# Kernel optimization log

Measured on AMD Instinct MI355X. Metric: run time of the kernel, lower is better.

Reference implementation:

```python
import jax, jax.numpy as jnp
import numpy as np

P_SIZE = 5
NUM_HEAD = 8
GN_EPS = 1e-5
LRELU_SLOPE = 0.2


def conv1x1(w, x, b=None):
    # w: [out_c, in_c], x: [n, in_c, h, w]
    y = jnp.einsum('oc,nchw->nohw', w, x)
    if b is not None:
        y = y + b[None, :, None, None]
    return y


def bilinear_sample(feat, sx, sy):
    """grid_sample(mode='bilinear', padding_mode='zeros', align_corners=True).
    With align_corners=True the normalize/denormalize round-trip in
    deformation_grid/grid_sample is the identity, so sx,sy are raw pixel coords.
    feat: [n,c,H,W]; sx,sy: [n,P,H,W] -> out [n,c,P,H,W]."""
    n, c, H, W = feat.shape
    x0 = jnp.floor(sx)
    y0 = jnp.floor(sy)
    x1 = x0 + 1.0
    y1 = y0 + 1.0
    wx1 = sx - x0
    wx0 = 1.0 - wx1
    wy1 = sy - y0
    wy0 = 1.0 - wy1
    feat_flat = feat.reshape(n, c, H * W)

    def corner(xi, yi, wgt):
        valid = (xi >= 0) & (xi <= W - 1) & (yi >= 0) & (yi <= H - 1)
        xc = jnp.clip(xi, 0, W - 1).astype(jnp.int32)
        yc = jnp.clip(yi, 0, H - 1).astype(jnp.int32)
        idx = (yc * W + xc).reshape(n, -1)                      # [n, P*H*W]
        g = jnp.take_along_axis(feat_flat, idx[:, None, :], axis=2)  # [n,c,P*H*W]
        g = g.reshape(n, c, xi.shape[1], H, W)                  # [n,c,P,H,W]
        wm = (wgt * valid.astype(feat.dtype))[:, None]          # [n,1,P,H,W]
        return g * wm

    return (corner(x0, y0, wx0 * wy0) + corner(x1, y0, wx1 * wy0)
            + corner(x0, y1, wx0 * wy1) + corner(x1, y1, wx1 * wy1))


def sample_coords(deform_field, p_size):
    # deform_field: [n,2,h,w] -> absolute pixel coords sx, sy: [n, p^2, h, w]
    n, _, h, w = deform_field.shape
    padding = (p_size - 1) // 2
    shift = jnp.arange(p_size, dtype=deform_field.dtype) - padding
    shift_y, shift_x = jnp.meshgrid(shift, shift, indexing='ij')  # [p,p]
    shift_y = shift_y.reshape(-1, 1, 1)  # [p^2,1,1]
    shift_x = shift_x.reshape(-1, 1, 1)
    gy = jnp.arange(h, dtype=deform_field.dtype)[:, None]  # [h,1]
    gx = jnp.arange(w, dtype=deform_field.dtype)[None, :]  # [1,w]
    sx = gx[None] + shift_x + deform_field[:, None, 0]     # [n,p^2,h,w]
    sy = gy[None] + shift_y + deform_field[:, None, 1]
    return sx, sy


def setup_inputs() -> dict:
    key = jax.random.key(0)
    ks = jax.random.split(key, 12)
    n, c, h, w = 2, 128, 96, 96
    hid = 256
    s = 0.05
    return {
        'query': jax.random.normal(ks[0], (n, c, h, w), jnp.float32),
        'key': jax.random.normal(ks[1], (n, c, h, w), jnp.float32),
        'value': jax.random.normal(ks[2], (n, c, h, w), jnp.float32),
        'deform_field': jax.random.normal(ks[3], (n, 2, h, w), jnp.float32) * 2.0,
        'w_q': jax.random.normal(ks[4], (c, c), jnp.float32) * s,
        'w_k': jax.random.normal(ks[5], (c, c), jnp.float32) * s,
        'w_v': jax.random.normal(ks[6], (c, c), jnp.float32) * s,
        'w_fc': jax.random.normal(ks[7], (c, c), jnp.float32) * s,
        'mlp_w1': jax.random.normal(ks[8], (hid, c), jnp.float32) * s,
        'mlp_b1': jnp.zeros((hid,), jnp.float32),
        'mlp_w2': jax.random.normal(ks[9], (c, hid), jnp.float32) * s,
        'mlp_b2': jnp.zeros((c,), jnp.float32),
        'gn_gamma': jnp.ones((c,), jnp.float32),
        'gn_beta': jnp.zeros((c,), jnp.float32),
    }


def reference(query, key, value, deform_field, w_q, w_k, w_v, w_fc,
              mlp_w1, mlp_b1, mlp_w2, mlp_b2, gn_gamma, gn_beta):
    p2 = P_SIZE * P_SIZE
    n, c, h, w = query.shape
    d_k = c // NUM_HEAD

    q = conv1x1(w_q, query)   # [n,c,h,w]
    k = conv1x1(w_k, key)
    v = conv1x1(w_v, value)

    # deformable window sampling of keys/values
    sx, sy = sample_coords(deform_field, P_SIZE)      # [n,p^2,h,w]
    k_s = bilinear_sample(k, sx, sy)                  # [n,c,p^2,h,w]
    v_s = bilinear_sample(v, sx, sy)

    # split heads
    q = q.reshape(n, NUM_HEAD, d_k, h, w)
    k_s = k_s.reshape(n, NUM_HEAD, d_k, p2, h, w)
    v_s = v_s.reshape(n, NUM_HEAD, d_k, p2, h, w)

    scale = 1.0 / jnp.sqrt(jnp.asarray(d_k, q.dtype))
    attn = jnp.einsum('nedyx,nedpyx->neyxp', q * scale, k_s)   # [n,head,h,w,p^2]
    attn = jax.nn.softmax(attn, axis=-1)
    out = jnp.einsum('neyxp,nedpyx->nedyx', attn, v_s)          # [n,head,d_v,h,w]
    out = out.reshape(n, c, h, w)
    out = conv1x1(w_fc, out)

    # conv-MLP residual
    hdn = conv1x1(mlp_w1, out, mlp_b1)
    hdn = jnp.where(hdn >= 0, hdn, LRELU_SLOPE * hdn)
    out = out + conv1x1(mlp_w2, hdn, mlp_b2)

    # GroupNorm(1, feat_dim): normalize over (C,H,W) per sample, per-channel affine
    mean = jnp.mean(out, axis=(1, 2, 3), keepdims=True)
    var = jnp.mean(jnp.square(out - mean), axis=(1, 2, 3), keepdims=True)
    out = (out - mean) * jax.lax.rsqrt(var + GN_EPS)
    out = out * gn_gamma[None, :, None, None] + gn_beta[None, :, None, None]
    return out
```

## Files before the change

kernel.cpp:

```cpp
#include <hip/hip_runtime.h>
#include <cstddef>

constexpr int Cc = 128;
constexpr int Hh = 96;
constexpr int Ww = 96;
constexpr int HW = Hh * Ww;
constexpr int Nn = 2;

typedef __attribute__((ext_vector_type(2))) _Float16 f16x2;
typedef __attribute__((ext_vector_type(4))) _Float16 f16x4;
typedef __attribute__((ext_vector_type(8))) _Float16 f16x8;
typedef __attribute__((ext_vector_type(4))) float f32x4;

__device__ __forceinline__ float fdot2(f16x2 a, f16x2 b, float c) {
#if defined(__has_builtin) && __has_builtin(__builtin_amdgcn_fdot2)
    return __builtin_amdgcn_fdot2(a, b, c, false);
#else
    return (float)a[0] * (float)b[0] + (float)a[1] * (float)b[1] + c;
#endif
}

__global__ void __launch_bounds__(256)
wcvt_k(const float* __restrict__ wq, const float* __restrict__ wk,
       const float* __restrict__ wv, const float* __restrict__ wfc,
       const float* __restrict__ w1, const float* __restrict__ w2,
       _Float16* __restrict__ dst)
{
    const int h0 = (blockIdx.x * 256 + threadIdx.x) * 8;
    const float* src; int off, K;
    if (h0 < 16384)      { src = wq;  off = h0;          K = 128; }
    else if (h0 < 32768) { src = wk;  off = h0 - 16384;  K = 128; }
    else if (h0 < 49152) { src = wv;  off = h0 - 32768;  K = 128; }
    else if (h0 < 65536) { src = wfc; off = h0 - 49152;  K = 128; }
    else if (h0 < 98304) { src = w1;  off = h0 - 65536;  K = 128; }
    else                 { src = w2;  off = h0 - 98304;  K = 256; }
    const int fid  = off >> 3;
    const int lane = fid & 63;
    const int n16  = lane & 15, quad = lane >> 4;
    const int t2   = fid >> 6;
    const int kcN  = K / 32;
    const int kc   = t2 % kcN;
    const int mt   = t2 / kcN;
    const int row  = mt * 16 + n16;
    const int col  = kc * 32 + quad * 8;
    const float* s = src + (size_t)row * K + col;
    const float4 a = *(const float4*)s;
    const float4 b = *(const float4*)(s + 4);
    f16x8 h = {(_Float16)a.x, (_Float16)a.y, (_Float16)a.z, (_Float16)a.w,
               (_Float16)b.x, (_Float16)b.y, (_Float16)b.z, (_Float16)b.w};
    *(f16x8*)&dst[h0] = h;
}

__global__ void __launch_bounds__(128)
qkv_k(const float* __restrict__ Xq, const float* __restrict__ Xk,
      const float* __restrict__ Xv, const _Float16* __restrict__ w16,
      _Float16* __restrict__ q16, _Float16* __restrict__ k16,
      _Float16* __restrict__ v16)
{
    const int t  = blockIdx.y;
    const int p0 = blockIdx.x * 64;
    const int z  = blockIdx.z;
    const float* X = (t == 0) ? Xq : (t == 1) ? Xk : Xv;
    _Float16* Y    = (t == 0) ? q16 : (t == 1) ? k16 : v16;
    const _Float16* W = w16 + (size_t)t * 16384;

    __shared__ _Float16 xl[128][72];
    const int tid = threadIdx.x;
    {
        const int px4 = (tid & 15) * 4, kg = tid >> 4;
        const float* Xz = X + (size_t)z * Cc * HW + p0 + px4;
#pragma unroll
        for (int kk = 0; kk < 16; ++kk) {
            const int k = kk * 8 + kg;
            float4 a = *(const float4*)&Xz[(size_t)k * HW];
            f16x4 h = {(_Float16)a.x, (_Float16)a.y, (_Float16)a.z, (_Float16)a.w};
            *(f16x4*)&xl[k][px4] = h;
        }
    }
    __syncthreads();

    const int w = tid >> 6, lane = tid & 63;
    const int n16 = lane & 15, quad = lane >> 4;
    const int pw = w * 32;

    f16x8 A[2][4];
#pragma unroll
    for (int mi = 0; mi < 2; ++mi) {
        const int px = pw + mi * 16 + n16;
#pragma unroll
        for (int kcid = 0; kcid < 4; ++kcid) {
            f16x8 av;
#pragma unroll
            for (int j = 0; j < 8; ++j) av[j] = xl[kcid * 32 + quad * 8 + j][px];
            A[mi][kcid] = av;
        }
    }

#pragma unroll
    for (int half = 0; half < 2; ++half) {
        const int oc0 = half * 64;
        f32x4 acc[2][4];
#pragma unroll
        for (int mi = 0; mi < 2; ++mi)
#pragma unroll
            for (int ni = 0; ni < 4; ++ni) acc[mi][ni] = (f32x4)0.f;

#pragma unroll
        for (int kcid = 0; kcid < 4; ++kcid) {
            f16x8 B[4];
#pragma unroll
            for (int ni = 0; ni < 4; ++ni)
                B[ni] = *(const f16x8*)&W[(((half * 4 + ni) * 4 + kcid) * 64 + lane) * 8];
#pragma unroll
            for (int mi = 0; mi < 2; ++mi)
#pragma unroll
                for (int ni = 0; ni < 4; ++ni)
                    acc[mi][ni] = __builtin_amdgcn_mfma_f32_16x16x32_f16(
                        A[mi][kcid], B[ni], acc[mi][ni], 0, 0, 0);
        }

#pragma unroll
        for (int mi = 0; mi < 2; ++mi)
#pragma unroll
            for (int r = 0; r < 4; ++r) {
                const int pix = p0 + pw + mi * 16 + quad * 4 + r;
                const size_t base = ((size_t)z * HW + pix) * Cc + oc0;
#pragma unroll
                for (int ni = 0; ni < 4; ++ni)
                    Y[base + ni * 16 + n16] = (_Float16)acc[mi][ni][r];
            }
    }
}

__global__ void __launch_bounds__(256)
attn_k(const _Float16* __restrict__ q, const _Float16* __restrict__ k,
       const _Float16* __restrict__ v, const float* __restrict__ df,
       _Float16* __restrict__ out)
{
    const int blk = blockIdx.x;
    const int sw = (blk & 7) * (1152 / 8) + (blk >> 3);
    const int wv = sw * 4 + (threadIdx.x >> 6);
    const int lane = threadIdx.x & 63;
    const int gp = wv * 4 + (lane >> 4);
    const int b = gp / HW;
    const int pix = gp - b * HW;
    const int y = pix / Ww, x = pix - y * Ww;
    const int co = (lane & 15) * 8;

    const float dx = df[((size_t)b * 2 + 0) * HW + pix];
    const float dy = df[((size_t)b * 2 + 1) * HW + pix];
    const float flx = floorf(dx), fly = floorf(dy);
    const int bx = x - 2 + (int)flx;
    const int by = y - 2 + (int)fly;
    const float wx1 = dx - flx, wx0 = 1.f - wx1;
    const float wy1 = dy - fly, wy0 = 1.f - wy1;
    const float u00 = wy0 * wx0, u01 = wy0 * wx1, u10 = wy1 * wx0, u11 = wy1 * wx1;
    const float s00 = u00 * 0.25f, s01 = u01 * 0.25f,
                s10 = u10 * 0.25f, s11 = u11 * 0.25f;

    const f16x8 qv8 = *(const f16x8*)&q[((size_t)b * HW + pix) * Cc + co];
    const f16x2 q0 = {qv8[0], qv8[1]}, q1 = {qv8[2], qv8[3]},
                q2 = {qv8[4], qv8[5]}, q3 = {qv8[6], qv8[7]};

    const _Float16* kp = k + ((size_t)b * HW) * Cc + co;
    const _Float16* vp = v + ((size_t)b * HW) * Cc + co;

    const bool inb = (bx >= 0) & (by >= 0) & (bx <= Ww - 6) & (by <= Hh - 6);
    const int allin = __all(inb);

    float qk[36];
    if (allin) {
        const _Float16* kr = kp + (size_t)(by * Ww + bx) * Cc;
#pragma unroll
        for (int r = 0; r < 6; ++r) {
#pragma unroll
            for (int c = 0; c < 6; ++c) {
                const f16x8 kv = *(const f16x8*)&kr[c * Cc];
                f16x2 k0 = {kv[0], kv[1]}, k1 = {kv[2], kv[3]};
                f16x2 k2 = {kv[4], kv[5]}, k3 = {kv[6], kv[7]};
                float d = fdot2(q0, k0, 0.f);
                d = fdot2(q1, k1, d);
                d = fdot2(q2, k2, d);
                d = fdot2(q3, k3, d);
                qk[r * 6 + c] = d;
            }
            kr += Ww * Cc;
        }
    } else {
#pragma unroll
        for (int r = 0; r < 6; ++r) {
            const int yr = by + r;
            const bool rv = (yr >= 0) & (yr < Hh);
            const int yc = min(max(yr, 0), Hh - 1);
            const _Float16* kr = kp + (size_t)(yc * Ww) * Cc;
#pragma unroll
            for (int c = 0; c < 6; ++c) {
                const int xc = bx + c;
                const bool cv = rv & (xc >= 0) & (xc < Ww);
                const int xcc = min(max(xc, 0), Ww - 1);
                const f16x8 kv = *(const f16x8*)&kr[xcc * Cc];
                f16x2 k0 = {kv[0], kv[1]}, k1 = {kv[2], kv[3]};
                f16x2 k2 = {kv[4], kv[5]}, k3 = {kv[6], kv[7]};
                float d = fdot2(q0, k0, 0.f);
                d = fdot2(q1, k1, d);
                d = fdot2(q2, k2, d);
                d = fdot2(q3, k3, d);
                qk[r * 6 + c] = cv ? d : 0.f;
            }
        }
    }

    float a[25];
#pragma unroll
    for (int py = 0; py < 5; ++py)
#pragma unroll
        for (int px = 0; px < 5; ++px) {
            float tv = s00 * qk[py * 6 + px];
            tv = fmaf(s01, qk[py * 6 + px + 1], tv);
            tv = fmaf(s10, qk[(py + 1) * 6 + px], tv);
            tv = fmaf(s11, qk[(py + 1) * 6 + px + 1], tv);
            a[py * 5 + px] = tv;
        }
#pragma unroll
    for (int i = 0; i < 25; ++i) a[i] += __shfl_xor(a[i], 1, 64);

    float mx = a[0];
#pragma unroll
    for (int i = 1; i < 25; ++i) mx = fmaxf(mx, a[i]);
    float ssum = 0.f;
#pragma unroll
    for (int i = 0; i < 25; ++i) { a[i] = __expf(a[i] - mx); ssum += a[i]; }
    const float inv = 1.f / ssum;

    float tmp[6][5];
#pragma unroll
    for (int r = 0; r < 6; ++r)
#pragma unroll
        for (int px = 0; px < 5; ++px) {
            float tv = 0.f;
            if (r < 5)  tv = a[r * 5 + px] * wy0;
            if (r >= 1) tv = fmaf(a[(r - 1) * 5 + px], wy1, tv);
            tmp[r][px] = tv;
        }
    float wsum[36];
#pragma unroll
    for (int r = 0; r < 6; ++r)
#pragma unroll
        for (int c = 0; c < 6; ++c) {
            float tv = 0.f;
            if (c < 5)  tv = tmp[r][c] * wx0;
            if (c >= 1) tv = fmaf(tmp[r][c - 1], wx1, tv);
            wsum[r * 6 + c] = tv;
        }

    float o[8] = {0.f, 0.f, 0.f, 0.f, 0.f, 0.f, 0.f, 0.f};
    if (allin) {
        const _Float16* vr = vp + (size_t)(by * Ww + bx) * Cc;
#pragma unroll
        for (int r = 0; r < 6; ++r) {
#pragma unroll
            for (int c = 0; c < 6; ++c) {
                const f16x8 vv = *(const f16x8*)&vr[c * Cc];
                const float wgt = wsum[r * 6 + c];
#pragma unroll
                for (int j = 0; j < 8; ++j)
                    o[j] = fmaf(wgt, (float)vv[j], o[j]);
            }
            vr += Ww * Cc;
        }
    } else {
#pragma unroll
        for (int r = 0; r < 6; ++r) {
            const int yr = by + r;
            const bool rv = (yr >= 0) & (yr < Hh);
            const int yc = min(max(yr, 0), Hh - 1);
            const _Float16* vr = vp + (size_t)(yc * Ww) * Cc;
#pragma unroll
            for (int c = 0; c < 6; ++c) {
                const int xc = bx + c;
                const bool cv = rv & (xc >= 0) & (xc < Ww);
                const int xcc = min(max(xc, 0), Ww - 1);
                const f16x8 vv = *(const f16x8*)&vr[xcc * Cc];
                const float wgt = cv ? wsum[r * 6 + c] : 0.f;
#pragma unroll
                for (int j = 0; j < 8; ++j)
                    o[j] = fmaf(wgt, (float)vv[j], o[j]);
            }
        }
    }

    f16x8 ov;
#pragma unroll
    for (int j = 0; j < 8; ++j) ov[j] = (_Float16)(o[j] * inv);
    *(f16x8*)&out[((size_t)b * HW + pix) * Cc + co] = ov;
}

__global__ void __launch_bounds__(128)
fmlp_k(const _Float16* __restrict__ X, const _Float16* __restrict__ w16,
       const float* __restrict__ b1, const float* __restrict__ b2,
       float* __restrict__ y2, float* __restrict__ pb)
{
    __shared__ __align__(16) _Float16 y1l[32][136];
    __shared__ __align__(16) _Float16 hl[32][264];
    __shared__ float red[4];

    const int z  = blockIdx.z;
    const int p0 = blockIdx.x * 32;
    const int tid = threadIdx.x, w = tid >> 6, lane = tid & 63;
    const int n16 = lane & 15, quad = lane >> 4;
    const _Float16* Wfc = w16 + 49152;
    const _Float16* W1  = w16 + 65536;
    const _Float16* W2  = w16 + 98304;

    f32x4 acc1[2][4];
#pragma unroll
    for (int mi = 0; mi < 2; ++mi)
#pragma unroll
        for (int ni = 0; ni < 4; ++ni) acc1[mi][ni] = (f32x4)0.f;

    const _Float16* Xz = X + ((size_t)z * HW + p0) * 128;
#pragma unroll
    for (int kc = 0; kc < 4; ++kc) {
        f16x8 A[2], B[4];
#pragma unroll
        for (int mi = 0; mi < 2; ++mi)
            A[mi] = *(const f16x8*)&Xz[(size_t)(mi * 16 + n16) * 128 + kc * 32 + quad * 8];
#pragma unroll
        for (int ni = 0; ni < 4; ++ni)
            B[ni] = *(const f16x8*)&Wfc[(((w * 4 + ni) * 4 + kc) * 64 + lane) * 8];
#pragma unroll
        for (int mi = 0; mi < 2; ++mi)
#pragma unroll
            for (int ni = 0; ni < 4; ++ni)
                acc1[mi][ni] = __builtin_amdgcn_mfma_f32_16x16x32_f16(
                    A[mi], B[ni], acc1[mi][ni], 0, 0, 0);
    }
#pragma unroll
    for (int mi = 0; mi < 2; ++mi)
#pragma unroll
        for (int ni = 0; ni < 4; ++ni)
#pragma unroll
            for (int r = 0; r < 4; ++r)
                y1l[mi * 16 + quad * 4 + r][w * 64 + ni * 16 + n16] =
                    (_Float16)acc1[mi][ni][r];
    __syncthreads();

    f32x4 acc2[2][8];
#pragma unroll
    for (int mi = 0; mi < 2; ++mi)
#pragma unroll
        for (int ni = 0; ni < 8; ++ni) acc2[mi][ni] = (f32x4)0.f;

#pragma unroll
    for (int kc = 0; kc < 4; ++kc) {
        f16x8 A[2];
#pragma unroll
        for (int mi = 0; mi < 2; ++mi)
            A[mi] = *(const f16x8*)&y1l[mi * 16 + n16][kc * 32 + quad * 8];
#pragma unroll
        for (int ni = 0; ni < 8; ++ni) {
            const f16x8 B = *(const f16x8*)&W1[(((w * 8 + ni) * 4 + kc) * 64 + lane) * 8];
#pragma unroll
            for (int mi = 0; mi < 2; ++mi)
                acc2[mi][ni] = __builtin_amdgcn_mfma_f32_16x16x32_f16(
                    A[mi], B, acc2[mi][ni], 0, 0, 0);
        }
    }
    {
        float b1v[8];
#pragma unroll
        for (int ni = 0; ni < 8; ++ni) b1v[ni] = b1[w * 128 + ni * 16 + n16];
#pragma unroll
        for (int mi = 0; mi < 2; ++mi)
#pragma unroll
            for (int ni = 0; ni < 8; ++ni)
#pragma unroll
                for (int r = 0; r < 4; ++r) {
                    float tv = acc2[mi][ni][r] + b1v[ni];
                    tv = tv >= 0.f ? tv : 0.2f * tv;
                    hl[mi * 16 + quad * 4 + r][w * 128 + ni * 16 + n16] = (_Float16)tv;
                }
    }
    __syncthreads();

    f32x4 acc3[2][4];
#pragma unroll
    for (int mi = 0; mi < 2; ++mi)
#pragma unroll
        for (int ni = 0; ni < 4; ++ni) acc3[mi][ni] = (f32x4)0.f;

#pragma unroll
    for (int kc = 0; kc < 8; ++kc) {
        f16x8 A[2], B[4];
#pragma unroll
        for (int mi = 0; mi < 2; ++mi)
            A[mi] = *(const f16x8*)&hl[mi * 16 + n16][kc * 32 + quad * 8];
#pragma unroll
        for (int ni = 0; ni < 4; ++ni)
            B[ni] = *(const f16x8*)&W2[(((w * 4 + ni) * 8 + kc) * 64 + lane) * 8];
#pragma unroll
        for (int mi = 0; mi < 2; ++mi)
#pragma unroll
            for (int ni = 0; ni < 4; ++ni)
                acc3[mi][ni] = __builtin_amdgcn_mfma_f32_16x16x32_f16(
                    A[mi], B[ni], acc3[mi][ni], 0, 0, 0);
    }

    float b2v[4];
#pragma unroll
    for (int ni = 0; ni < 4; ++ni) b2v[ni] = b2[w * 64 + ni * 16 + n16];

    float lsum = 0.f, lsq = 0.f;
#pragma unroll
    for (int mi = 0; mi < 2; ++mi)
#pragma unroll
        for (int r = 0; r < 4; ++r) {
            const int pix = p0 + mi * 16 + quad * 4 + r;
            float* yp = &y2[((size_t)z * HW + pix) * 128 + w * 64];
#pragma unroll
            for (int ni = 0; ni < 4; ++ni) {
                float tv = acc3[mi][ni][r] + b2v[ni] + acc1[mi][ni][r];
                lsum += tv; lsq += tv * tv;
                yp[ni * 16 + n16] = tv;
            }
        }

#pragma unroll
    for (int m = 1; m < 64; m <<= 1) {
        lsum += __shfl_xor(lsum, m, 64);
        lsq  += __shfl_xor(lsq,  m, 64);
    }
    if (lane == 0) { red[w * 2] = lsum; red[w * 2 + 1] = lsq; }
    __syncthreads();
    if (tid == 0) {
        const int bid = blockIdx.z * gridDim.x + blockIdx.x;
        pb[bid * 2 + 0] = red[0] + red[2];
        pb[bid * 2 + 1] = red[1] + red[3];
    }
}

__global__ void __launch_bounds__(256)
gn_k(const float* __restrict__ y2, const float* __restrict__ pb,
     const float* __restrict__ gamma, const float* __restrict__ beta,
     float* __restrict__ out, const int nPerZ)
{
    __shared__ float t[32][68];
    __shared__ float redm[8];
    __shared__ float stats[2];
    const int z = blockIdx.z, c0 = blockIdx.y * 32, p0 = blockIdx.x * 64;
    const int tid = threadIdx.x;

    {
        float s = 0.f, qq = 0.f;
        for (int p = tid; p < nPerZ; p += 256) {
            s  += pb[(z * nPerZ + p) * 2 + 0];
            qq += pb[(z * nPerZ + p) * 2 + 1];
        }
#pragma unroll
        for (int m = 1; m < 64; m <<= 1) {
            s  += __shfl_xor(s,  m, 64);
            qq += __shfl_xor(qq, m, 64);
        }
        if ((tid & 63) == 0) {
            redm[(tid >> 6) * 2]     = s;
            redm[(tid >> 6) * 2 + 1] = qq;
        }
    }
    {
        const int px = tid >> 2, cq = tid & 3;
        const float* src = &y2[((size_t)z * HW + p0 + px) * Cc + c0 + cq * 8];
        const float4 a = *(const float4*)src;
        const float4 bq = *(const float4*)(src + 4);
        t[cq * 8 + 0][px] = a.x;  t[cq * 8 + 1][px] = a.y;
        t[cq * 8 + 2][px] = a.z;  t[cq * 8 + 3][px] = a.w;
        t[cq * 8 + 4][px] = bq.x; t[cq * 8 + 5][px] = bq.y;
        t[cq * 8 + 6][px] = bq.z; t[cq * 8 + 7][px] = bq.w;
    }
    __syncthreads();
    if (tid == 0) {
        const float invN = 1.f / (float)(Cc * HW);
        const float S = redm[0] + redm[2] + redm[4] + redm[6];
        const float Q = redm[1] + redm[3] + redm[5] + redm[7];
        const float mean = S * invN;
        const float var  = fmaf(-mean, mean, Q * invN);
        stats[0] = mean;
        stats[1] = rsqrtf(var + 1e-5f);
    }
    __syncthreads();
    {
        const float mean = stats[0], rs = stats[1];
        const int c = tid >> 3, pq = tid & 7;
        const float g = gamma[c0 + c] * rs, be = beta[c0 + c];
        float4 o1, o2;
        o1.x = fmaf(t[c][pq * 8 + 0] - mean, g, be);
        o1.y = fmaf(t[c][pq * 8 + 1] - mean, g, be);
        o1.z = fmaf(t[c][pq * 8 + 2] - mean, g, be);
        o1.w = fmaf(t[c][pq * 8 + 3] - mean, g, be);
        o2.x = fmaf(t[c][pq * 8 + 4] - mean, g, be);
        o2.y = fmaf(t[c][pq * 8 + 5] - mean, g, be);
        o2.z = fmaf(t[c][pq * 8 + 6] - mean, g, be);
        o2.w = fmaf(t[c][pq * 8 + 7] - mean, g, be);
        float* dst = &out[((size_t)z * Cc + c0 + c) * HW + p0 + pq * 8];
        *(float4*)dst = o1;
        *(float4*)(dst + 4) = o2;
    }
}

extern "C" void kernel_launch(void* const* d_in, const int* in_sizes, int n_in,
                              void* d_out, int out_size, void* d_ws, size_t ws_size,
                              hipStream_t stream)
{
    const float* query  = (const float*)d_in[0];
    const float* key    = (const float*)d_in[1];
    const float* value  = (const float*)d_in[2];
    const float* deform = (const float*)d_in[3];
    const float* w_q    = (const float*)d_in[4];
    const float* w_k    = (const float*)d_in[5];
    const float* w_v    = (const float*)d_in[6];
    const float* w_fc   = (const float*)d_in[7];
    const float* mlp_w1 = (const float*)d_in[8];
    const float* mlp_b1 = (const float*)d_in[9];
    const float* mlp_w2 = (const float*)d_in[10];
    const float* mlp_b2 = (const float*)d_in[11];
    const float* gn_g   = (const float*)d_in[12];
    const float* gn_b   = (const float*)d_in[13];
    float* out = (float*)d_out;

    char* wsb = (char*)d_ws;
    _Float16* w16 = (_Float16*)wsb;
    float* pb   = (float*)(wsb + 262144);
    _Float16* T = (_Float16*)(wsb + 524288);
    const size_t S16 = (size_t)Nn * HW * Cc;
    _Float16* q16  = T;
    _Float16* k16  = T + S16;
    _Float16* v16  = T + 2 * S16;
    _Float16* at16 = T + 3 * S16;
    float*    y2   = (float*)T;

    wcvt_k<<<dim3(64), dim3(256), 0, stream>>>(
        w_q, w_k, w_v, w_fc, mlp_w1, mlp_w2, w16);

    qkv_k<<<dim3(HW / 64, 3, Nn), dim3(128), 0, stream>>>(
        query, key, value, w16, q16, k16, v16);

    attn_k<<<dim3(Nn * HW / 16), dim3(256), 0, stream>>>(
        q16, k16, v16, deform, at16);

    fmlp_k<<<dim3(HW / 32, 1, Nn), dim3(128), 0, stream>>>(
        at16, w16, mlp_b1, mlp_b2, y2, pb);

    gn_k<<<dim3(HW / 64, Cc / 32, Nn), dim3(256), 0, stream>>>(
        y2, pb, gn_g, gn_b, out, HW / 32);
}
```

Baseline: 150.0 us.

## Fuse Q projection, deformable attention and MLP into one kernel with fp16 output

The Q projection moves out of the QKV kernel into a new fused kernel that computes Q in shared memory, runs the per-pixel deformable attention, then does the fc and MLP GEMMs. This avoids writing and rereading the q16 and attention-output tensors in global memory and drops one kernel launch. The MLP result y2 is now stored as fp16 instead of fp32, halving its traffic into the GroupNorm kernel at some cost in precision. Blocks grow to 512 threads with a swizzled tile order, and each wave now owns a smaller slice of output channels in the GEMMs.

```diff
diff --git a/kernel.cpp b/kernel.cpp
--- a/kernel.cpp
+++ b/kernel.cpp
@@ -52,17 +52,16 @@
 }
 
 __global__ void __launch_bounds__(128)
-qkv_k(const float* __restrict__ Xq, const float* __restrict__ Xk,
-      const float* __restrict__ Xv, const _Float16* __restrict__ w16,
-      _Float16* __restrict__ q16, _Float16* __restrict__ k16,
-      _Float16* __restrict__ v16)
+kv_k(const float* __restrict__ Xk, const float* __restrict__ Xv,
+     const _Float16* __restrict__ w16,
+     _Float16* __restrict__ k16, _Float16* __restrict__ v16)
 {
     const int t  = blockIdx.y;
     const int p0 = blockIdx.x * 64;
     const int z  = blockIdx.z;
-    const float* X = (t == 0) ? Xq : (t == 1) ? Xk : Xv;
-    _Float16* Y    = (t == 0) ? q16 : (t == 1) ? k16 : v16;
-    const _Float16* W = w16 + (size_t)t * 16384;
+    const float* X = (t == 0) ? Xk : Xv;
+    _Float16* Y    = (t == 0) ? k16 : v16;
+    const _Float16* W = w16 + 16384 + (size_t)t * 16384;
 
     __shared__ _Float16 xl[128][72];
     const int tid = threadIdx.x;
@@ -132,297 +131,305 @@
     }
 }
 
-__global__ void __launch_bounds__(256)
-attn_k(const _Float16* __restrict__ q, const _Float16* __restrict__ k,
-       const _Float16* __restrict__ v, const float* __restrict__ df,
-       _Float16* __restrict__ out)
+__global__ void __launch_bounds__(512)
+qaf_k(const float* __restrict__ Xq, const _Float16* __restrict__ w16,
+      const _Float16* __restrict__ k16, const _Float16* __restrict__ v16,
+      const float* __restrict__ df, const float* __restrict__ b1,
+      const float* __restrict__ b2, _Float16* __restrict__ y2,
+      float* __restrict__ pb)
 {
-    const int blk = blockIdx.x;
-    const int sw = (blk & 7) * (1152 / 8) + (blk >> 3);
-    const int wv = sw * 4 + (threadIdx.x >> 6);
-    const int lane = threadIdx.x & 63;
-    const int gp = wv * 4 + (lane >> 4);
-    const int b = gp / HW;
-    const int pix = gp - b * HW;
-    const int y = pix / Ww, x = pix - y * Ww;
-    const int co = (lane & 15) * 8;
-
-    const float dx = df[((size_t)b * 2 + 0) * HW + pix];
-    const float dy = df[((size_t)b * 2 + 1) * HW + pix];
-    const float flx = floorf(dx), fly = floorf(dy);
-    const int bx = x - 2 + (int)flx;
-    const int by = y - 2 + (int)fly;
-    const float wx1 = dx - flx, wx0 = 1.f - wx1;
-    const float wy1 = dy - fly, wy0 = 1.f - wy1;
-    const float u00 = wy0 * wx0, u01 = wy0 * wx1, u10 = wy1 * wx0, u11 = wy1 * wx1;
-    const float s00 = u00 * 0.25f, s01 = u01 * 0.25f,
-                s10 = u10 * 0.25f, s11 = u11 * 0.25f;
-
-    const f16x8 qv8 = *(const f16x8*)&q[((size_t)b * HW + pix) * Cc + co];
-    const f16x2 q0 = {qv8[0], qv8[1]}, q1 = {qv8[2], qv8[3]},
-                q2 = {qv8[4], qv8[5]}, q3 = {qv8[6], qv8[7]};
-
-    const _Float16* kp = k + ((size_t)b * HW) * Cc + co;
-    const _Float16* vp = v + ((size_t)b * HW) * Cc + co;
-
-    const bool inb = (bx >= 0) & (by >= 0) & (bx <= Ww - 6) & (by <= Hh - 6);
-    const int allin = __all(inb);
-
-    float qk[36];
-    if (allin) {
-        const _Float16* kr = kp + (size_t)(by * Ww + bx) * Cc;
-#pragma unroll
-        for (int r = 0; r < 6; ++r) {
-#pragma unroll
-            for (int c = 0; c < 6; ++c) {
-                const f16x8 kv = *(const f16x8*)&kr[c * Cc];
-                f16x2 k0 = {kv[0], kv[1]}, k1 = {kv[2], kv[3]};
-                f16x2 k2 = {kv[4], kv[5]}, k3 = {kv[6], kv[7]};
-                float d = fdot2(q0, k0, 0.f);
-                d = fdot2(q1, k1, d);
-                d = fdot2(q2, k2, d);
-                d = fdot2(q3, k3, d);
-                qk[r * 6 + c] = d;
-            }
-            kr += Ww * Cc;
-        }
-    } else {
-#pragma unroll
-        for (int r = 0; r < 6; ++r) {
-            const int yr = by + r;
-            const bool rv = (yr >= 0) & (yr < Hh);
-            const int yc = min(max(yr, 0), Hh - 1);
-            const _Float16* kr = kp + (size_t)(yc * Ww) * Cc;
-#pragma unroll
-            for (int c = 0; c < 6; ++c) {
-                const int xc = bx + c;
-                const bool cv = rv & (xc >= 0) & (xc < Ww);
-                const int xcc = min(max(xc, 0), Ww - 1);
-                const f16x8 kv = *(const f16x8*)&kr[xcc * Cc];
-                f16x2 k0 = {kv[0], kv[1]}, k1 = {kv[2], kv[3]};
-                f16x2 k2 = {kv[4], kv[5]}, k3 = {kv[6], kv[7]};
-                float d = fdot2(q0, k0, 0.f);
-                d = fdot2(q1, k1, d);
-                d = fdot2(q2, k2, d);
-                d = fdot2(q3, k3, d);
-                qk[r * 6 + c] = cv ? d : 0.f;
-            }
-        }
-    }
-
-    float a[25];
-#pragma unroll
-    for (int py = 0; py < 5; ++py)
-#pragma unroll
-        for (int px = 0; px < 5; ++px) {
-            float tv = s00 * qk[py * 6 + px];
-            tv = fmaf(s01, qk[py * 6 + px + 1], tv);
-            tv = fmaf(s10, qk[(py + 1) * 6 + px], tv);
-            tv = fmaf(s11, qk[(py + 1) * 6 + px + 1], tv);
-            a[py * 5 + px] = tv;
-        }
-#pragma unroll
-    for (int i = 0; i < 25; ++i) a[i] += __shfl_xor(a[i], 1, 64);
-
-    float mx = a[0];
-#pragma unroll
-    for (int i = 1; i < 25; ++i) mx = fmaxf(mx, a[i]);
-    float ssum = 0.f;
-#pragma unroll
-    for (int i = 0; i < 25; ++i) { a[i] = __expf(a[i] - mx); ssum += a[i]; }
-    const float inv = 1.f / ssum;
-
-    float tmp[6][5];
-#pragma unroll
-    for (int r = 0; r < 6; ++r)
-#pragma unroll
-        for (int px = 0; px < 5; ++px) {
-            float tv = 0.f;
-            if (r < 5)  tv = a[r * 5 + px] * wy0;
-            if (r >= 1) tv = fmaf(a[(r - 1) * 5 + px], wy1, tv);
-            tmp[r][px] = tv;
-        }
-    float wsum[36];
-#pragma unroll
-    for (int r = 0; r < 6; ++r)
-#pragma unroll
-        for (int c = 0; c < 6; ++c) {
-            float tv = 0.f;
-            if (c < 5)  tv = tmp[r][c] * wx0;
-            if (c >= 1) tv = fmaf(tmp[r][c - 1], wx1, tv);
-            wsum[r * 6 + c] = tv;
-        }
-
-    float o[8] = {0.f, 0.f, 0.f, 0.f, 0.f, 0.f, 0.f, 0.f};
-    if (allin) {
-        const _Float16* vr = vp + (size_t)(by * Ww + bx) * Cc;
-#pragma unroll
-        for (int r = 0; r < 6; ++r) {
-#pragma unroll
-            for (int c = 0; c < 6; ++c) {
-                const f16x8 vv = *(const f16x8*)&vr[c * Cc];
-                const float wgt = wsum[r * 6 + c];
-#pragma unroll
-                for (int j = 0; j < 8; ++j)
-                    o[j] = fmaf(wgt, (float)vv[j], o[j]);
-            }
-            vr += Ww * Cc;
-        }
-    } else {
-#pragma unroll
-        for (int r = 0; r < 6; ++r) {
-            const int yr = by + r;
-            const bool rv = (yr >= 0) & (yr < Hh);
-            const int yc = min(max(yr, 0), Hh - 1);
-            const _Float16* vr = vp + (size_t)(yc * Ww) * Cc;
-#pragma unroll
-            for (int c = 0; c < 6; ++c) {
-                const int xc = bx + c;
-                const bool cv = rv & (xc >= 0) & (xc < Ww);
-                const int xcc = min(max(xc, 0), Ww - 1);
-                const f16x8 vv = *(const f16x8*)&vr[xcc * Cc];
-                const float wgt = cv ? wsum[r * 6 + c] : 0.f;
-#pragma unroll
-                for (int j = 0; j < 8; ++j)
-                    o[j] = fmaf(wgt, (float)vv[j], o[j]);
-            }
-        }
-    }
-
-    f16x8 ov;
-#pragma unroll
-    for (int j = 0; j < 8; ++j) ov[j] = (_Float16)(o[j] * inv);
-    *(f16x8*)&out[((size_t)b * HW + pix) * Cc + co] = ov;
-}
-
-__global__ void __launch_bounds__(128)
-fmlp_k(const _Float16* __restrict__ X, const _Float16* __restrict__ w16,
-       const float* __restrict__ b1, const float* __restrict__ b2,
-       float* __restrict__ y2, float* __restrict__ pb)
-{
+    __shared__ __align__(16) _Float16 xl[128][40];
+    __shared__ __align__(16) _Float16 ql[32][136];
     __shared__ __align__(16) _Float16 y1l[32][136];
     __shared__ __align__(16) _Float16 hl[32][264];
-    __shared__ float red[4];
+    __shared__ float red[16];
 
     const int z  = blockIdx.z;
-    const int p0 = blockIdx.x * 32;
+    const int bx = blockIdx.x;
+    const int ti = (bx & 7) * 36 + (bx >> 3);
+    const int p0 = ti * 32;
     const int tid = threadIdx.x, w = tid >> 6, lane = tid & 63;
     const int n16 = lane & 15, quad = lane >> 4;
+
+    {
+        const int px4 = (tid & 7) * 4, k0 = tid >> 3;
+        const float* Xz = Xq + (size_t)z * Cc * HW + p0 + px4;
+#pragma unroll
+        for (int kk = 0; kk < 2; ++kk) {
+            const int k = kk * 64 + k0;
+            float4 a = *(const float4*)&Xz[(size_t)k * HW];
+            f16x4 h4 = {(_Float16)a.x, (_Float16)a.y, (_Float16)a.z, (_Float16)a.w};
+            *(f16x4*)&xl[k][px4] = h4;
+        }
+    }
+    __syncthreads();
+
+    {
+        f32x4 qa[2];
+        qa[0] = (f32x4)0.f; qa[1] = (f32x4)0.f;
+#pragma unroll
+        for (int kc = 0; kc < 4; ++kc) {
+            f16x8 A[2];
+#pragma unroll
+            for (int mi = 0; mi < 2; ++mi) {
+                f16x8 av;
+#pragma unroll
+                for (int j = 0; j < 8; ++j)
+                    av[j] = xl[kc * 32 + quad * 8 + j][mi * 16 + n16];
+                A[mi] = av;
+            }
+            const f16x8 B = *(const f16x8*)&w16[((w * 4 + kc) * 64 + lane) * 8];
+#pragma unroll
+            for (int mi = 0; mi < 2; ++mi)
+                qa[mi] = __builtin_amdgcn_mfma_f32_16x16x32_f16(A[mi], B, qa[mi], 0, 0, 0);
+        }
+#pragma unroll
+        for (int mi = 0; mi < 2; ++mi)
+#pragma unroll
+            for (int r = 0; r < 4; ++r)
+                ql[mi * 16 + quad * 4 + r][w * 16 + n16] = (_Float16)qa[mi][r];
+    }
+    __syncthreads();
+
+    {
+        const int lpx = w * 4 + (lane >> 4);
+        const int pix = p0 + lpx;
+        const int y = pix / Ww, x = pix - y * Ww;
+        const int co = n16 * 8;
+
+        const float dx = df[((size_t)z * 2 + 0) * HW + pix];
+        const float dy = df[((size_t)z * 2 + 1) * HW + pix];
+        const float flx = floorf(dx), fly = floorf(dy);
+        const int bxp = x - 2 + (int)flx;
+        const int byp = y - 2 + (int)fly;
+        const float wx1 = dx - flx, wx0 = 1.f - wx1;
+        const float wy1 = dy - fly, wy0 = 1.f - wy1;
+        const float s00 = wy0 * wx0 * 0.25f, s01 = wy0 * wx1 * 0.25f,
+                    s10 = wy1 * wx0 * 0.25f, s11 = wy1 * wx1 * 0.25f;
+
+        const f16x8 qv8 = *(const f16x8*)&ql[lpx][co];
+        const f16x2 q0 = {qv8[0], qv8[1]}, q1 = {qv8[2], qv8[3]},
+                    q2 = {qv8[4], qv8[5]}, q3 = {qv8[6], qv8[7]};
+
+        const _Float16* kp = k16 + ((size_t)z * HW) * Cc + co;
+        const _Float16* vp = v16 + ((size_t)z * HW) * Cc + co;
+
+        const bool inb = (bxp >= 0) & (byp >= 0) & (bxp <= Ww - 6) & (byp <= Hh - 6);
+        const int allin = __all(inb);
+
+        float qk[36];
+        if (allin) {
+            const _Float16* kr = kp + (size_t)(byp * Ww + bxp) * Cc;
+#pragma unroll
+            for (int r = 0; r < 6; ++r) {
+#pragma unroll
+                for (int c = 0; c < 6; ++c) {
+                    const f16x8 kv = *(const f16x8*)&kr[c * Cc];
+                    f16x2 k0 = {kv[0], kv[1]}, k1 = {kv[2], kv[3]};
+                    f16x2 k2 = {kv[4], kv[5]}, k3 = {kv[6], kv[7]};
+                    float d = fdot2(q0, k0, 0.f);
+                    d = fdot2(q1, k1, d);
+                    d = fdot2(q2, k2, d);
+                    d = fdot2(q3, k3, d);
+                    qk[r * 6 + c] = d;
+                }
+                kr += Ww * Cc;
+            }
+        } else {
+#pragma unroll
+            for (int r = 0; r < 6; ++r) {
+                const int yr = byp + r;
+                const bool rv = (yr >= 0) & (yr < Hh);
+                const int yc = min(max(yr, 0), Hh - 1);
+                const _Float16* kr = kp + (size_t)(yc * Ww) * Cc;
+#pragma unroll
+                for (int c = 0; c < 6; ++c) {
+                    const int xc = bxp + c;
+                    const bool cv = rv & (xc >= 0) & (xc < Ww);
+                    const int xcc = min(max(xc, 0), Ww - 1);
+                    const f16x8 kv = *(const f16x8*)&kr[xcc * Cc];
+                    f16x2 k0 = {kv[0], kv[1]}, k1 = {kv[2], kv[3]};
+                    f16x2 k2 = {kv[4], kv[5]}, k3 = {kv[6], kv[7]};
+                    float d = fdot2(q0, k0, 0.f);
+                    d = fdot2(q1, k1, d);
+                    d = fdot2(q2, k2, d);
+                    d = fdot2(q3, k3, d);
+                    qk[r * 6 + c] = cv ? d : 0.f;
+                }
+            }
+        }
+
+        float a[25];
+#pragma unroll
+        for (int py = 0; py < 5; ++py)
+#pragma unroll
+            for (int px = 0; px < 5; ++px) {
+                float tv = s00 * qk[py * 6 + px];
+                tv = fmaf(s01, qk[py * 6 + px + 1], tv);
+                tv = fmaf(s10, qk[(py + 1) * 6 + px], tv);
+                tv = fmaf(s11, qk[(py + 1) * 6 + px + 1], tv);
+                a[py * 5 + px] = tv;
+            }
+#pragma unroll
+        for (int i = 0; i < 25; ++i) a[i] += __shfl_xor(a[i], 1, 64);
+
+        float mx = a[0];
+#pragma unroll
+        for (int i = 1; i < 25; ++i) mx = fmaxf(mx, a[i]);
+        float ssum = 0.f;
+#pragma unroll
+        for (int i = 0; i < 25; ++i) { a[i] = __expf(a[i] - mx); ssum += a[i]; }
+        const float inv = 1.f / ssum;
+
+        float tmp[6][5];
+#pragma unroll
+        for (int r = 0; r < 6; ++r)
+#pragma unroll
+            for (int px = 0; px < 5; ++px) {
+                float tv = 0.f;
+                if (r < 5)  tv = a[r * 5 + px] * wy0;
+                if (r >= 1) tv = fmaf(a[(r - 1) * 5 + px], wy1, tv);
+                tmp[r][px] = tv;
+            }
+        float wsum[36];
+#pragma unroll
+        for (int r = 0; r < 6; ++r)
+#pragma unroll
+            for (int c = 0; c < 6; ++c) {
+                float tv = 0.f;
+                if (c < 5)  tv = tmp[r][c] * wx0;
+                if (c >= 1) tv = fmaf(tmp[r][c - 1], wx1, tv);
+                wsum[r * 6 + c] = tv;
+            }
+
+        float o[8] = {0.f, 0.f, 0.f, 0.f, 0.f, 0.f, 0.f, 0.f};
+        if (allin) {
+            const _Float16* vr = vp + (size_t)(byp * Ww + bxp) * Cc;
+#pragma unroll
+            for (int r = 0; r < 6; ++r) {
+#pragma unroll
+                for (int c = 0; c < 6; ++c) {
+                    const f16x8 vv = *(const f16x8*)&vr[c * Cc];
+                    const float wgt = wsum[r * 6 + c];
+#pragma unroll
+                    for (int j = 0; j < 8; ++j)
+                        o[j] = fmaf(wgt, (float)vv[j], o[j]);
+                }
+                vr += Ww * Cc;
+            }
+        } else {
+#pragma unroll
+            for (int r = 0; r < 6; ++r) {
+                const int yr = byp + r;
+                const bool rv = (yr >= 0) & (yr < Hh);
+                const int yc = min(max(yr, 0), Hh - 1);
+                const _Float16* vr = vp + (size_t)(yc * Ww) * Cc;
+#pragma unroll
+                for (int c = 0; c < 6; ++c) {
+                    const int xc = bxp + c;
+                    const bool cv = rv & (xc >= 0) & (xc < Ww);
+                    const int xcc = min(max(xc, 0), Ww - 1);
+                    const f16x8 vv = *(const f16x8*)&vr[xcc * Cc];
+                    const float wgt = cv ? wsum[r * 6 + c] : 0.f;
+#pragma unroll
+                    for (int j = 0; j < 8; ++j)
+                        o[j] = fmaf(wgt, (float)vv[j], o[j]);
+                }
+            }
+        }
+
+        f16x8 ov;
+#pragma unroll
+        for (int j = 0; j < 8; ++j) ov[j] = (_Float16)(o[j] * inv);
+        *(f16x8*)&ql[lpx][co] = ov;
+    }
+    __syncthreads();
+
     const _Float16* Wfc = w16 + 49152;
     const _Float16* W1  = w16 + 65536;
     const _Float16* W2  = w16 + 98304;
 
-    f32x4 acc1[2][4];
-#pragma unroll
-    for (int mi = 0; mi < 2; ++mi)
-#pragma unroll
-        for (int ni = 0; ni < 4; ++ni) acc1[mi][ni] = (f32x4)0.f;
-
-    const _Float16* Xz = X + ((size_t)z * HW + p0) * 128;
-#pragma unroll
-    for (int kc = 0; kc < 4; ++kc) {
-        f16x8 A[2], B[4];
-#pragma unroll
-        for (int mi = 0; mi < 2; ++mi)
-            A[mi] = *(const f16x8*)&Xz[(size_t)(mi * 16 + n16) * 128 + kc * 32 + quad * 8];
-#pragma unroll
-        for (int ni = 0; ni < 4; ++ni)
-            B[ni] = *(const f16x8*)&Wfc[(((w * 4 + ni) * 4 + kc) * 64 + lane) * 8];
-#pragma unroll
-        for (int mi = 0; mi < 2; ++mi)
-#pragma unroll
-            for (int ni = 0; ni < 4; ++ni)
-                acc1[mi][ni] = __builtin_amdgcn_mfma_f32_16x16x32_f16(
-                    A[mi], B[ni], acc1[mi][ni], 0, 0, 0);
-    }
-#pragma unroll
-    for (int mi = 0; mi < 2; ++mi)
-#pragma unroll
-        for (int ni = 0; ni < 4; ++ni)
-#pragma unroll
-            for (int r = 0; r < 4; ++r)
-                y1l[mi * 16 + quad * 4 + r][w * 64 + ni * 16 + n16] =
-                    (_Float16)acc1[mi][ni][r];
-    __syncthreads();
-
-    f32x4 acc2[2][8];
-#pragma unroll
-    for (int mi = 0; mi < 2; ++mi)
-#pragma unroll
-        for (int ni = 0; ni < 8; ++ni) acc2[mi][ni] = (f32x4)0.f;
-
+    f32x4 acc1[2];
+    acc1[0] = (f32x4)0.f; acc1[1] = (f32x4)0.f;
 #pragma unroll
     for (int kc = 0; kc < 4; ++kc) {
         f16x8 A[2];
 #pragma unroll
         for (int mi = 0; mi < 2; ++mi)
-            A[mi] = *(const f16x8*)&y1l[mi * 16 + n16][kc * 32 + quad * 8];
-#pragma unroll
-        for (int ni = 0; ni < 8; ++ni) {
-            const f16x8 B = *(const f16x8*)&W1[(((w * 8 + ni) * 4 + kc) * 64 + lane) * 8];
+            A[mi] = *(const f16x8*)&ql[mi * 16 + n16][kc * 32 + quad * 8];
+        const f16x8 B = *(const f16x8*)&Wfc[((w * 4 + kc) * 64 + lane) * 8];
+#pragma unroll
+        for (int mi = 0; mi < 2; ++mi)
+            acc1[mi] = __builtin_amdgcn_mfma_f32_16x16x32_f16(A[mi], B, acc1[mi], 0, 0, 0);
+    }
+#pragma unroll
+    for (int mi = 0; mi < 2; ++mi)
+#pragma unroll
+        for (int r = 0; r < 4; ++r)
+            y1l[mi * 16 + quad * 4 + r][w * 16 + n16] = (_Float16)acc1[mi][r];
+    __syncthreads();
+
+    {
+        f32x4 acc2[2][2];
+#pragma unroll
+        for (int mi = 0; mi < 2; ++mi)
+#pragma unroll
+            for (int ni = 0; ni < 2; ++ni) acc2[mi][ni] = (f32x4)0.f;
+#pragma unroll
+        for (int kc = 0; kc < 4; ++kc) {
+            f16x8 A[2];
 #pragma unroll
             for (int mi = 0; mi < 2; ++mi)
-                acc2[mi][ni] = __builtin_amdgcn_mfma_f32_16x16x32_f16(
-                    A[mi], B, acc2[mi][ni], 0, 0, 0);
-        }
-    }
-    {
-        float b1v[8];
-#pragma unroll
-        for (int ni = 0; ni < 8; ++ni) b1v[ni] = b1[w * 128 + ni * 16 + n16];
-#pragma unroll
-        for (int mi = 0; mi < 2; ++mi)
-#pragma unroll
-            for (int ni = 0; ni < 8; ++ni)
+                A[mi] = *(const f16x8*)&y1l[mi * 16 + n16][kc * 32 + quad * 8];
+#pragma unroll
+            for (int ni = 0; ni < 2; ++ni) {
+                const f16x8 B = *(const f16x8*)&W1[(((w * 2 + ni) * 4 + kc) * 64 + lane) * 8];
+#pragma unroll
+                for (int mi = 0; mi < 2; ++mi)
+                    acc2[mi][ni] = __builtin_amdgcn_mfma_f32_16x16x32_f16(
+                        A[mi], B, acc2[mi][ni], 0, 0, 0);
+            }
+        }
+        float b1v[2];
+#pragma unroll
+        for (int ni = 0; ni < 2; ++ni) b1v[ni] = b1[w * 32 + ni * 16 + n16];
+#pragma unroll
+        for (int mi = 0; mi < 2; ++mi)
+#pragma unroll
+            for (int ni = 0; ni < 2; ++ni)
 #pragma unroll
                 for (int r = 0; r < 4; ++r) {
                     float tv = acc2[mi][ni][r] + b1v[ni];
                     tv = tv >= 0.f ? tv : 0.2f * tv;
-                    hl[mi * 16 + quad * 4 + r][w * 128 + ni * 16 + n16] = (_Float16)tv;
+                    hl[mi * 16 + quad * 4 + r][w * 32 + ni * 16 + n16] = (_Float16)tv;
                 }
     }
     __syncthreads();
 
-    f32x4 acc3[2][4];
-#pragma unroll
-    for (int mi = 0; mi < 2; ++mi)
-#pragma unroll
-        for (int ni = 0; ni < 4; ++ni) acc3[mi][ni] = (f32x4)0.f;
-
+    f32x4 acc3[2];
+    acc3[0] = (f32x4)0.f; acc3[1] = (f32x4)0.f;
 #pragma unroll
     for (int kc = 0; kc < 8; ++kc) {
-        f16x8 A[2], B[4];
+        f16x8 A[2];
 #pragma unroll
         for (int mi = 0; mi < 2; ++mi)
             A[mi] = *(const f16x8*)&hl[mi * 16 + n16][kc * 32 + quad * 8];
-#pragma unroll
-        for (int ni = 0; ni < 4; ++ni)
-            B[ni] = *(const f16x8*)&W2[(((w * 4 + ni) * 8 + kc) * 64 + lane) * 8];
-#pragma unroll
-        for (int mi = 0; mi < 2; ++mi)
-#pragma unroll
-            for (int ni = 0; ni < 4; ++ni)
-                acc3[mi][ni] = __builtin_amdgcn_mfma_f32_16x16x32_f16(
-                    A[mi], B[ni], acc3[mi][ni], 0, 0, 0);
-    }
-
-    float b2v[4];
-#pragma unroll
-    for (int ni = 0; ni < 4; ++ni) b2v[ni] = b2[w * 64 + ni * 16 + n16];
-
+        const f16x8 B = *(const f16x8*)&W2[((w * 8 + kc) * 64 + lane) * 8];
+#pragma unroll
+        for (int mi = 0; mi < 2; ++mi)
+            acc3[mi] = __builtin_amdgcn_mfma_f32_16x16x32_f16(A[mi], B, acc3[mi], 0, 0, 0);
+    }
+
+    const float b2v = b2[w * 16 + n16];
     float lsum = 0.f, lsq = 0.f;
 #pragma unroll
     for (int mi = 0; mi < 2; ++mi)
 #pragma unroll
         for (int r = 0; r < 4; ++r) {
             const int pix = p0 + mi * 16 + quad * 4 + r;
-            float* yp = &y2[((size_t)z * HW + pix) * 128 + w * 64];
-#pragma unroll
-            for (int ni = 0; ni < 4; ++ni) {
-                float tv = acc3[mi][ni][r] + b2v[ni] + acc1[mi][ni][r];
-                lsum += tv; lsq += tv * tv;
-                yp[ni * 16 + n16] = tv;
-            }
+            const float tv = acc3[mi][r] + b2v + acc1[mi][r];
+            lsum += tv; lsq += tv * tv;
+            y2[((size_t)z * HW + pix) * Cc + w * 16 + n16] = (_Float16)tv;
         }
 
 #pragma unroll
@@ -433,14 +440,17 @@
     if (lane == 0) { red[w * 2] = lsum; red[w * 2 + 1] = lsq; }
     __syncthreads();
     if (tid == 0) {
-        const int bid = blockIdx.z * gridDim.x + blockIdx.x;
-        pb[bid * 2 + 0] = red[0] + red[2];
-        pb[bid * 2 + 1] = red[1] + red[3];
+        float S = 0.f, Q = 0.f;
+#pragma unroll
+        for (int i = 0; i < 8; ++i) { S += red[i * 2]; Q += red[i * 2 + 1]; }
+        const int bid = z * (HW / 32) + bx;
+        pb[bid * 2 + 0] = S;
+        pb[bid * 2 + 1] = Q;
     }
 }
 
 __global__ void __launch_bounds__(256)
-gn_k(const float* __restrict__ y2, const float* __restrict__ pb,
+gn_k(const _Float16* __restrict__ y2, const float* __restrict__ pb,
      const float* __restrict__ gamma, const float* __restrict__ beta,
      float* __restrict__ out, const int nPerZ)
 {
@@ -468,13 +478,9 @@
     }
     {
         const int px = tid >> 2, cq = tid & 3;
-        const float* src = &y2[((size_t)z * HW + p0 + px) * Cc + c0 + cq * 8];
-        const float4 a = *(const float4*)src;
-        const float4 bq = *(const float4*)(src + 4);
-        t[cq * 8 + 0][px] = a.x;  t[cq * 8 + 1][px] = a.y;
-        t[cq * 8 + 2][px] = a.z;  t[cq * 8 + 3][px] = a.w;
-        t[cq * 8 + 4][px] = bq.x; t[cq * 8 + 5][px] = bq.y;
-        t[cq * 8 + 6][px] = bq.z; t[cq * 8 + 7][px] = bq.w;
+        const f16x8 a = *(const f16x8*)&y2[((size_t)z * HW + p0 + px) * Cc + c0 + cq * 8];
+#pragma unroll
+        for (int j = 0; j < 8; ++j) t[cq * 8 + j][px] = (float)a[j];
     }
     __syncthreads();
     if (tid == 0) {
@@ -531,24 +537,19 @@
     float* pb   = (float*)(wsb + 262144);
     _Float16* T = (_Float16*)(wsb + 524288);
     const size_t S16 = (size_t)Nn * HW * Cc;
-    _Float16* q16  = T;
-    _Float16* k16  = T + S16;
-    _Float16* v16  = T + 2 * S16;
-    _Float16* at16 = T + 3 * S16;
-    float*    y2   = (float*)T;
+    _Float16* k16  = T;
+    _Float16* v16  = T + S16;
+    _Float16* y2h  = T + 2 * S16;
 
     wcvt_k<<<dim3(64), dim3(256), 0, stream>>>(
         w_q, w_k, w_v, w_fc, mlp_w1, mlp_w2, w16);
 
-    qkv_k<<<dim3(HW / 64, 3, Nn), dim3(128), 0, stream>>>(
-        query, key, value, w16, q16, k16, v16);
-
-    attn_k<<<dim3(Nn * HW / 16), dim3(256), 0, stream>>>(
-        q16, k16, v16, deform, at16);
-
-    fmlp_k<<<dim3(HW / 32, 1, Nn), dim3(128), 0, stream>>>(
-        at16, w16, mlp_b1, mlp_b2, y2, pb);
+    kv_k<<<dim3(HW / 64, 2, Nn), dim3(128), 0, stream>>>(
+        key, value, w16, k16, v16);
+
+    qaf_k<<<dim3(HW / 32, 1, Nn), dim3(512), 0, stream>>>(
+        query, w16, k16, v16, deform, mlp_b1, mlp_b2, y2h, pb);
 
     gn_k<<<dim3(HW / 64, Cc / 32, Nn), dim3(256), 0, stream>>>(
-        y2, pb, gn_g, gn_b, out, HW / 32);
+        y2h, pb, gn_g, gn_b, out, HW / 32);
 }
```

Measured after the change: 147.8 us. Within noise of the previous version (-1.5%).
